# Performance work log

Hardware: AMD Instinct MI355X
Metric: run time of the kernel (lower is better)

The kernel has to match this reference:

```python
import jax, jax.numpy as jnp
import numpy as np

NU = 160000   # users
NM = 60000    # movies
D = 64        # embedding dim
E = 5000000   # rating edges
L = 200000    # label edges to score
NUM_LAYERS = 3


def setup_inputs() -> dict:
    key = jax.random.key(0)
    k1, k2, k3, k4, k5, k6 = jax.random.split(key, 6)
    return {
        "emb_user": jax.random.normal(k1, (NU, D), jnp.float32),
        "emb_movie": jax.random.normal(k2, (NM, D), jnp.float32),
        "node_id_user": jnp.arange(NU),
        "node_id_movie": jnp.arange(NM),
        "edge_from": jax.random.randint(k3, (E,), 0, NM),   # movie side of each edge
        "edge_to": jax.random.randint(k4, (E,), 0, NU),     # user side of each edge
        "label_movie": jax.random.randint(k5, (L,), 0, NM),
        "label_user": jax.random.randint(k6, (L,), 0, NU),
    }


def reference(emb_user, emb_movie, node_id_user, node_id_movie,
              edge_from, edge_to, label_movie, label_user):
    # Embedding lookup (node_id is an arange over all nodes in the batch)
    x_u = emb_user[node_id_user]    # [NU, D]
    x_m = emb_movie[node_id_movie]  # [NM, D]

    # Symmetric degree normalization: deg(from)^-1/2 * deg(to)^-1/2 per edge
    ones = jnp.ones(edge_from.shape[0], dtype=x_m.dtype)
    deg_m = jax.ops.segment_sum(ones, edge_from, num_segments=NM)
    deg_u = jax.ops.segment_sum(ones, edge_to, num_segments=NU)
    inv_m = jnp.where(deg_m > 0, deg_m ** -0.5, 0.0)
    inv_u = jnp.where(deg_u > 0, deg_u ** -0.5, 0.0)
    norm = inv_m[edge_from] * inv_u[edge_to]  # [E]

    # NOTE: the original torch code never writes the propagated embeddings back
    # into x_dict, so every layer propagates the layer-0 embeddings. Replicated
    # faithfully here.
    embs_u = [x_u]
    embs_m = [x_m]
    for _ in range(NUM_LAYERS):
        # movie -> user aggregation (x2y): gather movie feats, scale, scatter-add to users
        u_agg = jax.ops.segment_sum(norm[:, None] * x_m[edge_from], edge_to, num_segments=NU)
        m_agg = jax.ops.segment_sum(norm[:, None] * x_u[edge_to], edge_from, num_segments=NM)
        embs_u.append(u_agg)
        embs_m.append(m_agg)

    # Layer combination with weights 1/(l+1)
    w = 1.0 / (jnp.arange(NUM_LAYERS + 1, dtype=x_u.dtype) + 1.0)
    res_u = jnp.einsum('l,lnd->nd', w, jnp.stack(embs_u))  # [NU, D]
    res_m = jnp.einsum('l,lnd->nd', w, jnp.stack(embs_m))  # [NM, D]

    # Classifier: dot product over label edges
    scores = jnp.sum(res_u[label_user] * res_m[label_movie], axis=-1)  # [L]
    return (scores, res_u, res_m)
```

## Files before the change

### kernel.cpp

```cpp
#include <hip/hip_runtime.h>
#include <hip/hip_bf16.h>

#define NU 160000
#define NM 60000
#define DD 64
#define NE 5000000
#define NL 200000

#define COEF (13.0f / 12.0f)

#define SHIFT_U 9
#define SHIFT_M 7
#define NBU ((NU + (1 << SHIFT_U) - 1) >> SHIFT_U)
#define NBM ((NM + (1 << SHIFT_M) - 1) >> SHIFT_M)
#define VB_U 16
#define VB_M 18


#define CEC 16

__global__ void bucket_count_kernel(const int* __restrict__ ef, const int* __restrict__ et,
                                    int* __restrict__ gbh_u, int* __restrict__ gbh_m) {
    __shared__ int bhu[NBU], bhm[NBM];
    int tid = threadIdx.x;
    for (int i = tid; i < NBU; i += 256) bhu[i] = 0;
    for (int i = tid; i < NBM; i += 256) bhm[i] = 0;
    __syncthreads();
    int base = (blockIdx.x * 256 + tid) * CEC;
    if (base < NE) {
        const int4* f4 = (const int4*)(ef + base);
        const int4* t4 = (const int4*)(et + base);
        #pragma unroll
        for (int q = 0; q < CEC / 4; q++) {
            int4 ff = f4[q]; int4 tt = t4[q];
            atomicAdd(&bhm[ff.x >> SHIFT_M], 1); atomicAdd(&bhu[tt.x >> SHIFT_U], 1);
            atomicAdd(&bhm[ff.y >> SHIFT_M], 1); atomicAdd(&bhu[tt.y >> SHIFT_U], 1);
            atomicAdd(&bhm[ff.z >> SHIFT_M], 1); atomicAdd(&bhu[tt.z >> SHIFT_U], 1);
            atomicAdd(&bhm[ff.w >> SHIFT_M], 1); atomicAdd(&bhu[tt.w >> SHIFT_U], 1);
        }
    }
    __syncthreads();
    for (int i = tid; i < NBU; i += 256) if (bhu[i]) atomicAdd(&gbh_u[i], bhu[i]);
    for (int i = tid; i < NBM; i += 256) if (bhm[i]) atomicAdd(&gbh_m[i], bhm[i]);
}


__global__ void scan_small_kernel(const int* __restrict__ in, int* __restrict__ out,
                                  int* __restrict__ cur, int n) {
    __shared__ int buf[256];
    int tid = threadIdx.x;
    int idx = tid * 4;
    int v0 = (idx + 0 < n) ? in[idx + 0] : 0;
    int v1 = (idx + 1 < n) ? in[idx + 1] : 0;
    int v2 = (idx + 2 < n) ? in[idx + 2] : 0;
    int v3 = (idx + 3 < n) ? in[idx + 3] : 0;
    int s = v0 + v1 + v2 + v3;
    buf[tid] = s;
    __syncthreads();
    for (int off = 1; off < 256; off <<= 1) {
        int t = (tid >= off) ? buf[tid - off] : 0;
        __syncthreads();
        buf[tid] += t;
        __syncthreads();
    }
    int p = buf[tid] - s;
    if (idx + 0 < n) { out[idx + 0] = p; if (cur) cur[idx + 0] = p; p += v0; }
    if (idx + 1 < n) { out[idx + 1] = p; if (cur) cur[idx + 1] = p; p += v1; }
    if (idx + 2 < n) { out[idx + 2] = p; if (cur) cur[idx + 2] = p; p += v2; }
    if (idx + 3 < n) { out[idx + 3] = p; if (cur) cur[idx + 3] = p; p += v3; }
    if (tid == 255) out[n] = buf[255];
}


#define PEC 16

__global__ void partition_kernel(const int* __restrict__ key, const int* __restrict__ val,
                                 int* __restrict__ bcur, int* __restrict__ stage,
                                 int shift, int nb, int valbits) {
    __shared__ int lh[512];
    __shared__ int lbase[512];
    int tid = threadIdx.x;
    int lmask = (1 << shift) - 1;
    for (int i = tid; i < nb; i += 256) lh[i] = 0;
    __syncthreads();
    int base = (blockIdx.x * 256 + tid) * PEC;
    int k_[PEC], v_[PEC], br_[PEC];
    bool act = base < NE;
    if (act) {
        const int4* k4 = (const int4*)(key + base);
        const int4* v4 = (const int4*)(val + base);
        #pragma unroll
        for (int q = 0; q < PEC / 4; q++) {
            int4 kk = k4[q]; int4 vv = v4[q];
            k_[q * 4 + 0] = kk.x; k_[q * 4 + 1] = kk.y; k_[q * 4 + 2] = kk.z; k_[q * 4 + 3] = kk.w;
            v_[q * 4 + 0] = vv.x; v_[q * 4 + 1] = vv.y; v_[q * 4 + 2] = vv.z; v_[q * 4 + 3] = vv.w;
        }
        #pragma unroll
        for (int q = 0; q < PEC; q++) {
            int b = k_[q] >> shift;
            int r = atomicAdd(&lh[b], 1);
            br_[q] = (b << 13) | r;
        }
    }
    __syncthreads();
    for (int i = tid; i < nb; i += 256) lbase[i] = lh[i] ? atomicAdd(&bcur[i], lh[i]) : 0;
    __syncthreads();
    if (act) {
        #pragma unroll
        for (int q = 0; q < PEC; q++) {
            int b = br_[q] >> 13;
            int r = br_[q] & 8191;
            stage[lbase[b] + r] = ((k_[q] & lmask) << valbits) | v_[q];
        }
    }
}


__global__ void build_kernel(const int* __restrict__ stage, const int* __restrict__ bo,
                             float* __restrict__ inv, int* __restrict__ rp,
                             int* __restrict__ pay, int shift, int n, int valbits) {
    __shared__ int cnt[512];
    __shared__ int tmp[512];
    int b = blockIdx.x;
    int tid = threadIdx.x;
    int bs = 1 << shift;
    int base = b << shift;
    int nn = min(bs, n - base);
    int vmask = (1 << valbits) - 1;
    int s0 = bo[b];
    int s1 = bo[b + 1];

    for (int i = tid; i < bs; i += 256) cnt[i] = 0;
    __syncthreads();
    for (int e = s0 + tid; e < s1; e += 256)
        atomicAdd(&cnt[stage[e] >> valbits], 1);
    __syncthreads();
    int o0 = (tid < bs) ? cnt[tid] : 0;
    int o1 = (tid + 256 < bs) ? cnt[tid + 256] : 0;
    for (int off = 1; off < bs; off <<= 1) {
        for (int i = tid; i < bs; i += 256) tmp[i] = (i >= off) ? cnt[i - off] : 0;
        __syncthreads();
        for (int i = tid; i < bs; i += 256) cnt[i] += tmp[i];
        __syncthreads();
    }
    if (tid < bs) {
        int excl = cnt[tid] - o0;
        tmp[tid] = s0 + excl;
        if (tid < nn) {
            rp[base + tid] = s0 + excl;
            inv[base + tid] = (o0 > 0) ? rsqrtf((float)o0) : 0.0f;
        }
    }
    if (tid + 256 < bs) {
        int i = tid + 256;
        int excl = cnt[i] - o1;
        tmp[i] = s0 + excl;
        if (i < nn) {
            rp[base + i] = s0 + excl;
            inv[base + i] = (o1 > 0) ? rsqrtf((float)o1) : 0.0f;
        }
    }
    if (b == 0 && tid == 0) rp[n] = NE;
    __syncthreads();
    for (int e = s0 + tid; e < s1; e += 256) {
        int p = stage[e];
        int pos = atomicAdd(&tmp[p >> valbits], 1);
        pay[pos] = p & vmask;
    }
}


__global__ void prescale_kernel(const float* __restrict__ x, const float* __restrict__ inv,
                                __hip_bfloat16* __restrict__ y, int total) {
    int i = blockIdx.x * blockDim.x + threadIdx.x;
    if (i < total) {
        int node = i >> 6;
        y[i] = __float2bfloat16(inv[node] * x[i]);
    }
}


__global__ void gather_kernel(const int* __restrict__ rp, const int* __restrict__ pay,
                              const float* __restrict__ inv_dst,
                              const __hip_bfloat16* __restrict__ y_src,
                              const float* __restrict__ x_dst,
                              float* __restrict__ res, int n) {
    int tid = blockIdx.x * blockDim.x + threadIdx.x;
    int node = tid >> 6;
    int lane = threadIdx.x & 63;
    if (node >= n) return;
    int start = rp[node];
    int end   = rp[node + 1];
    float acc = 0.0f;
    for (int i = start; i < end; i += 64) {
        int cnt = min(end - i, 64);
        int nid = (lane < cnt) ? pay[i + lane] : 0;
        int j = 0;
        for (; j + 4 <= cnt; j += 4) {
            int f0 = __shfl(nid, j + 0, 64);
            int f1 = __shfl(nid, j + 1, 64);
            int f2 = __shfl(nid, j + 2, 64);
            int f3 = __shfl(nid, j + 3, 64);
            float a0 = __bfloat162float(y_src[f0 * DD + lane]);
            float a1 = __bfloat162float(y_src[f1 * DD + lane]);
            float a2 = __bfloat162float(y_src[f2 * DD + lane]);
            float a3 = __bfloat162float(y_src[f3 * DD + lane]);
            acc += a0 + a1 + a2 + a3;
        }
        for (; j < cnt; j++) {
            int f0 = __shfl(nid, j, 64);
            acc += __bfloat162float(y_src[f0 * DD + lane]);
        }
    }
    int o = node * DD + lane;
    res[o] = x_dst[o] + COEF * inv_dst[node] * acc;
}


__global__ void score_kernel(const int* __restrict__ lm, const int* __restrict__ lu,
                             const float* __restrict__ ru, const float* __restrict__ rm,
                             float* __restrict__ scores) {
    int tid = blockIdx.x * blockDim.x + threadIdx.x;
    int l = tid >> 6;
    int d = threadIdx.x & 63;
    if (l < NL) {
        int u = lu[l];
        int m = lm[l];
        float v = ru[u * DD + d] * rm[m * DD + d];
        #pragma unroll
        for (int off = 32; off >= 1; off >>= 1)
            v += __shfl_down(v, off, 64);
        if (d == 0) scores[l] = v;
    }
}


__global__ void degree_kernel_f(const int* __restrict__ ef, const int* __restrict__ et,
                                float* __restrict__ deg_m, float* __restrict__ deg_u) {
    int i = blockIdx.x * blockDim.x + threadIdx.x;
    if (i < NE) {
        atomicAdd(&deg_m[ef[i]], 1.0f);
        atomicAdd(&deg_u[et[i]], 1.0f);
    }
}

__global__ void inv_kernel_f(float* __restrict__ deg, int n) {
    int i = blockIdx.x * blockDim.x + threadIdx.x;
    if (i < n) {
        float d = deg[i];
        deg[i] = (d > 0.0f) ? (1.0f / sqrtf(d)) : 0.0f;
    }
}

__global__ void agg_kernel_f(const int* __restrict__ ef, const int* __restrict__ et,
                             const float* __restrict__ inv_m, const float* __restrict__ inv_u,
                             const float* __restrict__ x_u, const float* __restrict__ x_m,
                             float* __restrict__ res_u, float* __restrict__ res_m) {
    int tid = blockIdx.x * blockDim.x + threadIdx.x;
    int e = tid >> 6;
    int d = tid & 63;
    if (e < NE) {
        int f = ef[e];
        int t = et[e];
        float norm = inv_m[f] * inv_u[t] * COEF;
        atomicAdd(&res_u[t * DD + d], norm * x_m[f * DD + d]);
        atomicAdd(&res_m[f * DD + d], norm * x_u[t * DD + d]);
    }
}

__global__ void add_base_kernel_f(const float* __restrict__ xu, const float* __restrict__ xm,
                                  float* __restrict__ ru, float* __restrict__ rm) {
    int i = blockIdx.x * blockDim.x + threadIdx.x;
    const int nu = NU * DD;
    const int nm = NM * DD;
    if (i < nu) {
        ru[i] += xu[i];
    } else if (i < nu + nm) {
        int j = i - nu;
        rm[j] += xm[j];
    }
}


extern "C" void kernel_launch(void* const* d_in, const int* in_sizes, int n_in,
                              void* d_out, int out_size, void* d_ws, size_t ws_size,
                              hipStream_t stream) {
    const float* emb_user  = (const float*)d_in[0];
    const float* emb_movie = (const float*)d_in[1];
    const int* edge_from   = (const int*)d_in[4];
    const int* edge_to     = (const int*)d_in[5];
    const int* label_movie = (const int*)d_in[6];
    const int* label_user  = (const int*)d_in[7];

    float* out    = (float*)d_out;
    float* scores = out;
    float* res_u  = out + NL;
    float* res_m  = out + NL + (size_t)NU * DD;

    int*   gbh_u  = (int*)d_ws;
    int*   gbh_m  = gbh_u + NBU;
    int*   bo_u   = gbh_m + NBM;
    int*   bcur_u = bo_u + NBU + 1;
    int*   bo_m   = bcur_u + NBU;
    int*   bcur_m = bo_m + NBM + 1;
    float* inv_u  = (float*)(bcur_m + NBM);
    float* inv_m  = inv_u + NU;
    int*   rp_u   = (int*)(inv_m + NM);
    int*   rp_m   = rp_u + NU + 1;
    int*   pay_u  = rp_m + NM + 1;
    int*   pay_m  = pay_u + NE;
    int*   ureg   = pay_m + NE;
    int*   stage  = ureg;
    __hip_bfloat16* y_u = (__hip_bfloat16*)ureg;
    __hip_bfloat16* y_m = (__hip_bfloat16*)(ureg + (size_t)NU * DD / 2);

    size_t ysz    = (size_t)(NU + NM) * DD / 2;
    size_t uni    = (size_t)NE > ysz ? (size_t)NE : ysz;
    size_t needed = ((size_t)(ureg - (int*)d_ws) + uni) * sizeof(int);

    if (ws_size >= needed) {
        hipMemsetAsync(gbh_u, 0, (size_t)(NBU + NBM) * sizeof(int), stream);

        bucket_count_kernel<<<(NE / CEC + 255) / 256, 256, 0, stream>>>(
            edge_from, edge_to, gbh_u, gbh_m);
        scan_small_kernel<<<1, 256, 0, stream>>>(gbh_u, bo_u, bcur_u, NBU);
        scan_small_kernel<<<1, 256, 0, stream>>>(gbh_m, bo_m, bcur_m, NBM);

        partition_kernel<<<(NE / PEC + 255) / 256, 256, 0, stream>>>(
            edge_to, edge_from, bcur_u, stage, SHIFT_U, NBU, VB_U);
        build_kernel<<<NBU, 256, 0, stream>>>(stage, bo_u, inv_u, rp_u, pay_u, SHIFT_U, NU, VB_U);

        partition_kernel<<<(NE / PEC + 255) / 256, 256, 0, stream>>>(
            edge_from, edge_to, bcur_m, stage, SHIFT_M, NBM, VB_M);
        build_kernel<<<NBM, 256, 0, stream>>>(stage, bo_m, inv_m, rp_m, pay_m, SHIFT_M, NM, VB_M);

        prescale_kernel<<<((size_t)NU * DD + 255) / 256, 256, 0, stream>>>(
            emb_user, inv_u, y_u, NU * DD);
        prescale_kernel<<<((size_t)NM * DD + 255) / 256, 256, 0, stream>>>(
            emb_movie, inv_m, y_m, NM * DD);

        gather_kernel<<<((size_t)NU * 64 + 255) / 256, 256, 0, stream>>>(
            rp_u, pay_u, inv_u, y_m, emb_user, res_u, NU);
        gather_kernel<<<((size_t)NM * 64 + 255) / 256, 256, 0, stream>>>(
            rp_m, pay_m, inv_m, y_u, emb_movie, res_m, NM);
    } else {
        float* fdeg_u = (float*)d_ws;
        float* fdeg_m = fdeg_u + NU;
        hipMemsetAsync(res_u, 0, (size_t)(NU + NM) * DD * sizeof(float), stream);
        hipMemsetAsync(fdeg_u, 0, (size_t)(NU + NM) * sizeof(float), stream);
        degree_kernel_f<<<(NE + 255) / 256, 256, 0, stream>>>(edge_from, edge_to, fdeg_m, fdeg_u);
        inv_kernel_f<<<(NU + NM + 255) / 256, 256, 0, stream>>>(fdeg_u, NU + NM);
        agg_kernel_f<<<((size_t)NE * 64 + 255) / 256, 256, 0, stream>>>(
            edge_from, edge_to, fdeg_m, fdeg_u, emb_user, emb_movie, res_u, res_m);
        add_base_kernel_f<<<((NU + NM) * DD + 255) / 256, 256, 0, stream>>>(
            emb_user, emb_movie, res_u, res_m);
    }

    score_kernel<<<((size_t)NL * 64 + 255) / 256, 256, 0, stream>>>(
        label_movie, label_user, res_u, res_m, scores);
}
```

Baseline: 717.1 us.

## Split CSR neighbor lists by source range and gather in cache-sized passes

Each destination node's adjacency list is sub-bucketed by which slice of the source embedding table the neighbor falls in: two slices for user destinations, six for movie destinations. The gather then runs one pass per slice, so each pass reads random rows from a source region small enough to stay resident in L2 rather than spilling to the larger last-level cache. Degree normalization is now derived from the expanded row pointers in a separate small kernel. The cost is extra kernel launches and repeated read-modify-write of the fp32 result rows across passes.

After: 798.5 us. 1.11x slower.

```diff
diff --git a/kernel.cpp b/kernel.cpp
--- a/kernel.cpp
+++ b/kernel.cpp
@@ -15,6 +15,16 @@
 #define NBM ((NM + (1 << SHIFT_M) - 1) >> SHIFT_M)
 #define VB_U 16
 #define VB_M 18
+
+#define UDIV 30000
+#define LG_U 1
+#define MDIV 27000
+#define LG_M 3
+#define NPASS_U 2
+#define NPASS_M 6
+#define NVU (NU << LG_U)
+#define NVM (NM << LG_M)
+#define BS 1024
 
 
 #define CEC 16
@@ -76,17 +86,17 @@
 
 __global__ void partition_kernel(const int* __restrict__ key, const int* __restrict__ val,
                                  int* __restrict__ bcur, int* __restrict__ stage,
-                                 int shift, int nb, int valbits) {
+                                 int nb, int valbits, int mode) {
     __shared__ int lh[512];
     __shared__ int lbase[512];
     int tid = threadIdx.x;
-    int lmask = (1 << shift) - 1;
     for (int i = tid; i < nb; i += 256) lh[i] = 0;
     __syncthreads();
     int base = (blockIdx.x * 256 + tid) * PEC;
-    int k_[PEC], v_[PEC], br_[PEC];
+    int kv_[PEC], v_[PEC], br_[PEC];
     bool act = base < NE;
     if (act) {
+        int k_[PEC];
         const int4* k4 = (const int4*)(key + base);
         const int4* v4 = (const int4*)(val + base);
         #pragma unroll
@@ -97,7 +107,11 @@
         }
         #pragma unroll
         for (int q = 0; q < PEC; q++) {
-            int b = k_[q] >> shift;
+            int kv;
+            if (mode == 0) kv = (k_[q] << LG_U) | (v_[q] >= UDIV ? 1 : 0);
+            else           kv = (k_[q] << LG_M) | (int)((unsigned)v_[q] / MDIV);
+            kv_[q] = kv;
+            int b = kv >> 10;
             int r = atomicAdd(&lh[b], 1);
             br_[q] = (b << 13) | r;
         }
@@ -110,55 +124,51 @@
         for (int q = 0; q < PEC; q++) {
             int b = br_[q] >> 13;
             int r = br_[q] & 8191;
-            stage[lbase[b] + r] = ((k_[q] & lmask) << valbits) | v_[q];
+            stage[lbase[b] + r] = ((kv_[q] & (BS - 1)) << valbits) | v_[q];
         }
     }
 }
 
 
 __global__ void build_kernel(const int* __restrict__ stage, const int* __restrict__ bo,
-                             float* __restrict__ inv, int* __restrict__ rp,
-                             int* __restrict__ pay, int shift, int n, int valbits) {
-    __shared__ int cnt[512];
-    __shared__ int tmp[512];
+                             int* __restrict__ rp, int* __restrict__ pay,
+                             int n, int valbits) {
+    __shared__ int cnt[BS];
+    __shared__ int tmp[BS];
     int b = blockIdx.x;
     int tid = threadIdx.x;
-    int bs = 1 << shift;
-    int base = b << shift;
-    int nn = min(bs, n - base);
+    int base = b << 10;
+    int nn = min(BS, n - base);
     int vmask = (1 << valbits) - 1;
     int s0 = bo[b];
     int s1 = bo[b + 1];
 
-    for (int i = tid; i < bs; i += 256) cnt[i] = 0;
+    for (int i = tid; i < BS; i += 256) cnt[i] = 0;
     __syncthreads();
     for (int e = s0 + tid; e < s1; e += 256)
         atomicAdd(&cnt[stage[e] >> valbits], 1);
     __syncthreads();
-    int o0 = (tid < bs) ? cnt[tid] : 0;
-    int o1 = (tid + 256 < bs) ? cnt[tid + 256] : 0;
-    for (int off = 1; off < bs; off <<= 1) {
-        for (int i = tid; i < bs; i += 256) tmp[i] = (i >= off) ? cnt[i - off] : 0;
+    int ov[4];
+    #pragma unroll
+    for (int q = 0; q < 4; q++) ov[q] = cnt[tid + q * 256];
+    for (int off = 1; off < BS; off <<= 1) {
+        int t[4];
+        #pragma unroll
+        for (int q = 0; q < 4; q++) {
+            int i = tid + q * 256;
+            t[q] = (i >= off) ? cnt[i - off] : 0;
+        }
         __syncthreads();
-        for (int i = tid; i < bs; i += 256) cnt[i] += tmp[i];
+        #pragma unroll
+        for (int q = 0; q < 4; q++) cnt[tid + q * 256] += t[q];
         __syncthreads();
     }
-    if (tid < bs) {
-        int excl = cnt[tid] - o0;
-        tmp[tid] = s0 + excl;
-        if (tid < nn) {
-            rp[base + tid] = s0 + excl;
-            inv[base + tid] = (o0 > 0) ? rsqrtf((float)o0) : 0.0f;
-        }
-    }
-    if (tid + 256 < bs) {
-        int i = tid + 256;
-        int excl = cnt[i] - o1;
+    #pragma unroll
+    for (int q = 0; q < 4; q++) {
+        int i = tid + q * 256;
+        int excl = cnt[i] - ov[q];
         tmp[i] = s0 + excl;
-        if (i < nn) {
-            rp[base + i] = s0 + excl;
-            inv[base + i] = (o1 > 0) ? rsqrtf((float)o1) : 0.0f;
-        }
+        if (i < nn) rp[base + i] = s0 + excl;
     }
     if (b == 0 && tid == 0) rp[n] = NE;
     __syncthreads();
@@ -170,6 +180,16 @@
 }
 
 
+__global__ void inv_from_rp_kernel(const int* __restrict__ rp, float* __restrict__ inv,
+                                   int n, int lg) {
+    int i = blockIdx.x * blockDim.x + threadIdx.x;
+    if (i < n) {
+        int d = rp[(i + 1) << lg] - rp[i << lg];
+        inv[i] = (d > 0) ? rsqrtf((float)d) : 0.0f;
+    }
+}
+
+
 __global__ void prescale_kernel(const float* __restrict__ x, const float* __restrict__ inv,
                                 __hip_bfloat16* __restrict__ y, int total) {
     int i = blockIdx.x * blockDim.x + threadIdx.x;
@@ -184,13 +204,15 @@
                               const float* __restrict__ inv_dst,
                               const __hip_bfloat16* __restrict__ y_src,
                               const float* __restrict__ x_dst,
-                              float* __restrict__ res, int n) {
+                              float* __restrict__ res, int n, int lg, int h, int first) {
     int tid = blockIdx.x * blockDim.x + threadIdx.x;
     int node = tid >> 6;
     int lane = threadIdx.x & 63;
     if (node >= n) return;
-    int start = rp[node];
-    int end   = rp[node + 1];
+    int vk = (node << lg) | h;
+    int start = rp[vk];
+    int end   = rp[vk + 1];
+    if (!first && start == end) return;
     float acc = 0.0f;
     for (int i = start; i < end; i += 64) {
         int cnt = min(end - i, 64);
@@ -213,7 +235,8 @@
         }
     }
     int o = node * DD + lane;
-    res[o] = x_dst[o] + COEF * inv_dst[node] * acc;
+    float basev = first ? x_dst[o] : res[o];
+    res[o] = basev + COEF * inv_dst[node] * acc;
 }
 
 
@@ -306,8 +329,8 @@
     float* inv_u  = (float*)(bcur_m + NBM);
     float* inv_m  = inv_u + NU;
     int*   rp_u   = (int*)(inv_m + NM);
-    int*   rp_m   = rp_u + NU + 1;
-    int*   pay_u  = rp_m + NM + 1;
+    int*   rp_m   = rp_u + NVU + 1;
+    int*   pay_u  = rp_m + NVM + 1;
     int*   pay_m  = pay_u + NE;
     int*   ureg   = pay_m + NE;
     int*   stage  = ureg;
@@ -327,22 +350,27 @@
         scan_small_kernel<<<1, 256, 0, stream>>>(gbh_m, bo_m, bcur_m, NBM);
 
         partition_kernel<<<(NE / PEC + 255) / 256, 256, 0, stream>>>(
-            edge_to, edge_from, bcur_u, stage, SHIFT_U, NBU, VB_U);
-        build_kernel<<<NBU, 256, 0, stream>>>(stage, bo_u, inv_u, rp_u, pay_u, SHIFT_U, NU, VB_U);
+            edge_to, edge_from, bcur_u, stage, NBU, VB_U, 0);
+        build_kernel<<<NBU, 256, 0, stream>>>(stage, bo_u, rp_u, pay_u, NVU, VB_U);
 
         partition_kernel<<<(NE / PEC + 255) / 256, 256, 0, stream>>>(
-            edge_from, edge_to, bcur_m, stage, SHIFT_M, NBM, VB_M);
-        build_kernel<<<NBM, 256, 0, stream>>>(stage, bo_m, inv_m, rp_m, pay_m, SHIFT_M, NM, VB_M);
+            edge_from, edge_to, bcur_m, stage, NBM, VB_M, 1);
+        build_kernel<<<NBM, 256, 0, stream>>>(stage, bo_m, rp_m, pay_m, NVM, VB_M);
+
+        inv_from_rp_kernel<<<(NU + 255) / 256, 256, 0, stream>>>(rp_u, inv_u, NU, LG_U);
+        inv_from_rp_kernel<<<(NM + 255) / 256, 256, 0, stream>>>(rp_m, inv_m, NM, LG_M);
 
         prescale_kernel<<<((size_t)NU * DD + 255) / 256, 256, 0, stream>>>(
             emb_user, inv_u, y_u, NU * DD);
         prescale_kernel<<<((size_t)NM * DD + 255) / 256, 256, 0, stream>>>(
             emb_movie, inv_m, y_m, NM * DD);
 
-        gather_kernel<<<((size_t)NU * 64 + 255) / 256, 256, 0, stream>>>(
-            rp_u, pay_u, inv_u, y_m, emb_user, res_u, NU);
-        gather_kernel<<<((size_t)NM * 64 + 255) / 256, 256, 0, stream>>>(
-            rp_m, pay_m, inv_m, y_u, emb_movie, res_m, NM);
+        for (int h = 0; h < NPASS_U; h++)
+            gather_kernel<<<((size_t)NU * 64 + 255) / 256, 256, 0, stream>>>(
+                rp_u, pay_u, inv_u, y_m, emb_user, res_u, NU, LG_U, h, h == 0);
+        for (int h = 0; h < NPASS_M; h++)
+            gather_kernel<<<((size_t)NM * 64 + 255) / 256, 256, 0, stream>>>(
+                rp_m, pay_m, inv_m, y_u, emb_movie, res_m, NM, LG_M, h, h == 0);
     } else {
         float* fdeg_u = (float*)d_ws;
         float* fdeg_m = fdeg_u + NU;
```

## Replace bucketed two-pass CSR build with global-atomic degree count and direct placement

Applied to the files above, without the earlier changes.

Replaces the bucket histogram, partition and per-bucket build kernels with a simpler CSR build. Per-node degrees are counted with global atomics, then a tiled scan produces row pointers, and a single place kernel scatters both user and movie payloads using atomic cursors. This cuts the number of passes over the edge list and drops the staging buffer. In exchange it relies on heavily contended global atomics and random scattered writes, and the order of edges within each row is no longer deterministic.

New measurement: 1.713 ms. 2.39x slower.

```diff
diff --git a/kernel.cpp b/kernel.cpp
--- a/kernel.cpp
+++ b/kernel.cpp
@@ -9,44 +9,56 @@
 
 #define COEF (13.0f / 12.0f)
 
-#define SHIFT_U 9
-#define SHIFT_M 7
-#define NBU ((NU + (1 << SHIFT_U) - 1) >> SHIFT_U)
-#define NBM ((NM + (1 << SHIFT_M) - 1) >> SHIFT_M)
-#define VB_U 16
-#define VB_M 18
-
 
 #define CEC 16
 
-__global__ void bucket_count_kernel(const int* __restrict__ ef, const int* __restrict__ et,
-                                    int* __restrict__ gbh_u, int* __restrict__ gbh_m) {
-    __shared__ int bhu[NBU], bhm[NBM];
-    int tid = threadIdx.x;
-    for (int i = tid; i < NBU; i += 256) bhu[i] = 0;
-    for (int i = tid; i < NBM; i += 256) bhm[i] = 0;
-    __syncthreads();
-    int base = (blockIdx.x * 256 + tid) * CEC;
+__global__ void deg_kernel(const int* __restrict__ ef, const int* __restrict__ et,
+                           int* __restrict__ deg_m, int* __restrict__ deg_u) {
+    int base = (blockIdx.x * 256 + threadIdx.x) * CEC;
     if (base < NE) {
         const int4* f4 = (const int4*)(ef + base);
         const int4* t4 = (const int4*)(et + base);
         #pragma unroll
         for (int q = 0; q < CEC / 4; q++) {
             int4 ff = f4[q]; int4 tt = t4[q];
-            atomicAdd(&bhm[ff.x >> SHIFT_M], 1); atomicAdd(&bhu[tt.x >> SHIFT_U], 1);
-            atomicAdd(&bhm[ff.y >> SHIFT_M], 1); atomicAdd(&bhu[tt.y >> SHIFT_U], 1);
-            atomicAdd(&bhm[ff.z >> SHIFT_M], 1); atomicAdd(&bhu[tt.z >> SHIFT_U], 1);
-            atomicAdd(&bhm[ff.w >> SHIFT_M], 1); atomicAdd(&bhu[tt.w >> SHIFT_U], 1);
+            atomicAdd(&deg_m[ff.x], 1); atomicAdd(&deg_u[tt.x], 1);
+            atomicAdd(&deg_m[ff.y], 1); atomicAdd(&deg_u[tt.y], 1);
+            atomicAdd(&deg_m[ff.z], 1); atomicAdd(&deg_u[tt.z], 1);
+            atomicAdd(&deg_m[ff.w], 1); atomicAdd(&deg_u[tt.w], 1);
         }
     }
+}
+
+
+__global__ void tile_scan_kernel(const int* __restrict__ in, int* __restrict__ rp,
+                                 int* __restrict__ tsum, int n) {
+    __shared__ int buf[256];
+    int tid = threadIdx.x;
+    int base = blockIdx.x * 1024;
+    int idx = base + tid * 4;
+    int v0 = (idx + 0 < n) ? in[idx + 0] : 0;
+    int v1 = (idx + 1 < n) ? in[idx + 1] : 0;
+    int v2 = (idx + 2 < n) ? in[idx + 2] : 0;
+    int v3 = (idx + 3 < n) ? in[idx + 3] : 0;
+    int s = v0 + v1 + v2 + v3;
+    buf[tid] = s;
     __syncthreads();
-    for (int i = tid; i < NBU; i += 256) if (bhu[i]) atomicAdd(&gbh_u[i], bhu[i]);
-    for (int i = tid; i < NBM; i += 256) if (bhm[i]) atomicAdd(&gbh_m[i], bhm[i]);
-}
-
-
-__global__ void scan_small_kernel(const int* __restrict__ in, int* __restrict__ out,
-                                  int* __restrict__ cur, int n) {
+    for (int off = 1; off < 256; off <<= 1) {
+        int t = (tid >= off) ? buf[tid - off] : 0;
+        __syncthreads();
+        buf[tid] += t;
+        __syncthreads();
+    }
+    int p = buf[tid] - s;
+    if (idx + 0 < n) { rp[idx + 0] = p; p += v0; }
+    if (idx + 1 < n) { rp[idx + 1] = p; p += v1; }
+    if (idx + 2 < n) { rp[idx + 2] = p; p += v2; }
+    if (idx + 3 < n) { rp[idx + 3] = p; }
+    if (tid == 255) tsum[blockIdx.x] = buf[255];
+}
+
+
+__global__ void scan_small_kernel(const int* __restrict__ in, int* __restrict__ out, int n) {
     __shared__ int buf[256];
     int tid = threadIdx.x;
     int idx = tid * 4;
@@ -64,108 +76,49 @@
         __syncthreads();
     }
     int p = buf[tid] - s;
-    if (idx + 0 < n) { out[idx + 0] = p; if (cur) cur[idx + 0] = p; p += v0; }
-    if (idx + 1 < n) { out[idx + 1] = p; if (cur) cur[idx + 1] = p; p += v1; }
-    if (idx + 2 < n) { out[idx + 2] = p; if (cur) cur[idx + 2] = p; p += v2; }
-    if (idx + 3 < n) { out[idx + 3] = p; if (cur) cur[idx + 3] = p; p += v3; }
+    if (idx + 0 < n) { out[idx + 0] = p; p += v0; }
+    if (idx + 1 < n) { out[idx + 1] = p; p += v1; }
+    if (idx + 2 < n) { out[idx + 2] = p; p += v2; }
+    if (idx + 3 < n) { out[idx + 3] = p; p += v3; }
     if (tid == 255) out[n] = buf[255];
 }
 
 
-#define PEC 16
-
-__global__ void partition_kernel(const int* __restrict__ key, const int* __restrict__ val,
-                                 int* __restrict__ bcur, int* __restrict__ stage,
-                                 int shift, int nb, int valbits) {
-    __shared__ int lh[512];
-    __shared__ int lbase[512];
-    int tid = threadIdx.x;
-    int lmask = (1 << shift) - 1;
-    for (int i = tid; i < nb; i += 256) lh[i] = 0;
-    __syncthreads();
-    int base = (blockIdx.x * 256 + tid) * PEC;
-    int k_[PEC], v_[PEC], br_[PEC];
-    bool act = base < NE;
-    if (act) {
-        const int4* k4 = (const int4*)(key + base);
-        const int4* v4 = (const int4*)(val + base);
+__global__ void scan_add_kernel(int* __restrict__ rp, const int* __restrict__ toff,
+                                const int* __restrict__ deg, float* __restrict__ inv,
+                                int* __restrict__ cur, int n) {
+    int i = blockIdx.x * blockDim.x + threadIdx.x;
+    if (i < n) {
+        int r = rp[i] + toff[i >> 10];
+        rp[i] = r;
+        cur[i] = r;
+        int d = deg[i];
+        inv[i] = (d > 0) ? rsqrtf((float)d) : 0.0f;
+        if (i == 0) rp[n] = NE;
+    }
+}
+
+
+__global__ void place_kernel(const int* __restrict__ ef, const int* __restrict__ et,
+                             int* __restrict__ cur_u, int* __restrict__ cur_m,
+                             int* __restrict__ pay_u, int* __restrict__ pay_m) {
+    int base = (blockIdx.x * 256 + threadIdx.x) * CEC;
+    if (base < NE) {
+        const int4* f4 = (const int4*)(ef + base);
+        const int4* t4 = (const int4*)(et + base);
         #pragma unroll
-        for (int q = 0; q < PEC / 4; q++) {
-            int4 kk = k4[q]; int4 vv = v4[q];
-            k_[q * 4 + 0] = kk.x; k_[q * 4 + 1] = kk.y; k_[q * 4 + 2] = kk.z; k_[q * 4 + 3] = kk.w;
-            v_[q * 4 + 0] = vv.x; v_[q * 4 + 1] = vv.y; v_[q * 4 + 2] = vv.z; v_[q * 4 + 3] = vv.w;
+        for (int q = 0; q < CEC / 4; q++) {
+            int4 ff = f4[q]; int4 tt = t4[q];
+            int p;
+            p = atomicAdd(&cur_u[tt.x], 1); pay_u[p] = ff.x;
+            p = atomicAdd(&cur_m[ff.x], 1); pay_m[p] = tt.x;
+            p = atomicAdd(&cur_u[tt.y], 1); pay_u[p] = ff.y;
+            p = atomicAdd(&cur_m[ff.y], 1); pay_m[p] = tt.y;
+            p = atomicAdd(&cur_u[tt.z], 1); pay_u[p] = ff.z;
+            p = atomicAdd(&cur_m[ff.z], 1); pay_m[p] = tt.z;
+            p = atomicAdd(&cur_u[tt.w], 1); pay_u[p] = ff.w;
+            p = atomicAdd(&cur_m[ff.w], 1); pay_m[p] = tt.w;
         }
-        #pragma unroll
-        for (int q = 0; q < PEC; q++) {
-            int b = k_[q] >> shift;
-            int r = atomicAdd(&lh[b], 1);
-            br_[q] = (b << 13) | r;
-        }
-    }
-    __syncthreads();
-    for (int i = tid; i < nb; i += 256) lbase[i] = lh[i] ? atomicAdd(&bcur[i], lh[i]) : 0;
-    __syncthreads();
-    if (act) {
-        #pragma unroll
-        for (int q = 0; q < PEC; q++) {
-            int b = br_[q] >> 13;
-            int r = br_[q] & 8191;
-            stage[lbase[b] + r] = ((k_[q] & lmask) << valbits) | v_[q];
-        }
-    }
-}
-
-
-__global__ void build_kernel(const int* __restrict__ stage, const int* __restrict__ bo,
-                             float* __restrict__ inv, int* __restrict__ rp,
-                             int* __restrict__ pay, int shift, int n, int valbits) {
-    __shared__ int cnt[512];
-    __shared__ int tmp[512];
-    int b = blockIdx.x;
-    int tid = threadIdx.x;
-    int bs = 1 << shift;
-    int base = b << shift;
-    int nn = min(bs, n - base);
-    int vmask = (1 << valbits) - 1;
-    int s0 = bo[b];
-    int s1 = bo[b + 1];
-
-    for (int i = tid; i < bs; i += 256) cnt[i] = 0;
-    __syncthreads();
-    for (int e = s0 + tid; e < s1; e += 256)
-        atomicAdd(&cnt[stage[e] >> valbits], 1);
-    __syncthreads();
-    int o0 = (tid < bs) ? cnt[tid] : 0;
-    int o1 = (tid + 256 < bs) ? cnt[tid + 256] : 0;
-    for (int off = 1; off < bs; off <<= 1) {
-        for (int i = tid; i < bs; i += 256) tmp[i] = (i >= off) ? cnt[i - off] : 0;
-        __syncthreads();
-        for (int i = tid; i < bs; i += 256) cnt[i] += tmp[i];
-        __syncthreads();
-    }
-    if (tid < bs) {
-        int excl = cnt[tid] - o0;
-        tmp[tid] = s0 + excl;
-        if (tid < nn) {
-            rp[base + tid] = s0 + excl;
-            inv[base + tid] = (o0 > 0) ? rsqrtf((float)o0) : 0.0f;
-        }
-    }
-    if (tid + 256 < bs) {
-        int i = tid + 256;
-        int excl = cnt[i] - o1;
-        tmp[i] = s0 + excl;
-        if (i < nn) {
-            rp[base + i] = s0 + excl;
-            inv[base + i] = (o1 > 0) ? rsqrtf((float)o1) : 0.0f;
-        }
-    }
-    if (b == 0 && tid == 0) rp[n] = NE;
-    __syncthreads();
-    for (int e = s0 + tid; e < s1; e += 256) {
-        int p = stage[e];
-        int pos = atomicAdd(&tmp[p >> valbits], 1);
-        pay[pos] = p & vmask;
     }
 }
 
@@ -297,42 +250,44 @@
     float* res_u  = out + NL;
     float* res_m  = out + NL + (size_t)NU * DD;
 
-    int*   gbh_u  = (int*)d_ws;
-    int*   gbh_m  = gbh_u + NBU;
-    int*   bo_u   = gbh_m + NBM;
-    int*   bcur_u = bo_u + NBU + 1;
-    int*   bo_m   = bcur_u + NBU;
-    int*   bcur_m = bo_m + NBM + 1;
-    float* inv_u  = (float*)(bcur_m + NBM);
+    const int NTU = (NU + 1023) >> 10;
+    const int NTM = (NM + 1023) >> 10;
+
+    int*   deg_u  = (int*)d_ws;
+    int*   deg_m  = deg_u + NU;
+    int*   rp_u   = deg_m + NM;
+    int*   rp_m   = rp_u + NU + 1;
+    int*   cur_u  = rp_m + NM + 1;
+    int*   cur_m  = cur_u + NU;
+    int*   tsum_u = cur_m + NM;
+    int*   toff_u = tsum_u + NTU;
+    int*   tsum_m = toff_u + NTU + 1;
+    int*   toff_m = tsum_m + NTM;
+    float* inv_u  = (float*)(toff_m + NTM + 1);
     float* inv_m  = inv_u + NU;
-    int*   rp_u   = (int*)(inv_m + NM);
-    int*   rp_m   = rp_u + NU + 1;
-    int*   pay_u  = rp_m + NM + 1;
+    int*   pay_u  = (int*)(inv_m + NM);
     int*   pay_m  = pay_u + NE;
-    int*   ureg   = pay_m + NE;
-    int*   stage  = ureg;
-    __hip_bfloat16* y_u = (__hip_bfloat16*)ureg;
-    __hip_bfloat16* y_m = (__hip_bfloat16*)(ureg + (size_t)NU * DD / 2);
+    __hip_bfloat16* y_u = (__hip_bfloat16*)(pay_m + NE);
+    __hip_bfloat16* y_m = y_u + (size_t)NU * DD;
 
     size_t ysz    = (size_t)(NU + NM) * DD / 2;
-    size_t uni    = (size_t)NE > ysz ? (size_t)NE : ysz;
-    size_t needed = ((size_t)(ureg - (int*)d_ws) + uni) * sizeof(int);
+    size_t needed = ((size_t)((int*)y_u - (int*)d_ws) + ysz) * sizeof(int);
 
     if (ws_size >= needed) {
-        hipMemsetAsync(gbh_u, 0, (size_t)(NBU + NBM) * sizeof(int), stream);
-
-        bucket_count_kernel<<<(NE / CEC + 255) / 256, 256, 0, stream>>>(
-            edge_from, edge_to, gbh_u, gbh_m);
-        scan_small_kernel<<<1, 256, 0, stream>>>(gbh_u, bo_u, bcur_u, NBU);
-        scan_small_kernel<<<1, 256, 0, stream>>>(gbh_m, bo_m, bcur_m, NBM);
-
-        partition_kernel<<<(NE / PEC + 255) / 256, 256, 0, stream>>>(
-            edge_to, edge_from, bcur_u, stage, SHIFT_U, NBU, VB_U);
-        build_kernel<<<NBU, 256, 0, stream>>>(stage, bo_u, inv_u, rp_u, pay_u, SHIFT_U, NU, VB_U);
-
-        partition_kernel<<<(NE / PEC + 255) / 256, 256, 0, stream>>>(
-            edge_from, edge_to, bcur_m, stage, SHIFT_M, NBM, VB_M);
-        build_kernel<<<NBM, 256, 0, stream>>>(stage, bo_m, inv_m, rp_m, pay_m, SHIFT_M, NM, VB_M);
+        hipMemsetAsync(deg_u, 0, (size_t)(NU + NM) * sizeof(int), stream);
+
+        deg_kernel<<<(NE / CEC + 255) / 256, 256, 0, stream>>>(
+            edge_from, edge_to, deg_m, deg_u);
+
+        tile_scan_kernel<<<NTU, 256, 0, stream>>>(deg_u, rp_u, tsum_u, NU);
+        tile_scan_kernel<<<NTM, 256, 0, stream>>>(deg_m, rp_m, tsum_m, NM);
+        scan_small_kernel<<<1, 256, 0, stream>>>(tsum_u, toff_u, NTU);
+        scan_small_kernel<<<1, 256, 0, stream>>>(tsum_m, toff_m, NTM);
+        scan_add_kernel<<<(NU + 255) / 256, 256, 0, stream>>>(rp_u, toff_u, deg_u, inv_u, cur_u, NU);
+        scan_add_kernel<<<(NM + 255) / 256, 256, 0, stream>>>(rp_m, toff_m, deg_m, inv_m, cur_m, NM);
+
+        place_kernel<<<(NE / CEC + 255) / 256, 256, 0, stream>>>(
+            edge_from, edge_to, cur_u, cur_m, pay_u, pay_m);
 
         prescale_kernel<<<((size_t)NU * DD + 255) / 256, 256, 0, stream>>>(
             emb_user, inv_u, y_u, NU * DD);
```
